# Performance work log

Hardware: AMD Instinct MI355X
Metric: run time of the kernel (lower is better)

Reference implementation:

```python
import jax, jax.numpy as jnp
import numpy as np

NUM_USER = 20000
NUM_ITEM = 40000
N_NODES = NUM_USER + NUM_ITEM
DIM = 64
V_DIM = 2048
T_DIM = 768
N_EDGES = 1_000_000
K_USER = 40
K_ITEM = 10
N_LAYERS = 2


def setup_inputs() -> dict:
    key = jax.random.key(0)
    ks = iter(jax.random.split(key, 32))

    def xavier(shape):
        s = (2.0 / (shape[0] + shape[-1])) ** 0.5
        return jax.random.normal(next(ks), shape, jnp.float32) * s

    # bipartite user-item interactions, doubled (undirected), as in DRAGON.__init__
    u = jax.random.randint(next(ks), (N_EDGES,), 0, NUM_USER)
    it = jax.random.randint(next(ks), (N_EDGES,), NUM_USER, N_NODES)
    edge_index = jnp.stack([jnp.concatenate([u, it]), jnp.concatenate([it, u])])

    v_feat = jax.random.normal(next(ks), (NUM_ITEM, V_DIM), jnp.float32)
    t_feat = jax.random.normal(next(ks), (NUM_ITEM, T_DIM), jnp.float32)

    # KNN item-item adjacency (top-10 per row) with symmetric-normalized values,
    # mirroring get_knn_adj_mat/compute_normalized_laplacian
    rows = jnp.repeat(jnp.arange(NUM_ITEM), K_ITEM)
    cols = jax.random.randint(next(ks), (NUM_ITEM * K_ITEM,), 0, NUM_ITEM)
    mm_indices = jnp.stack([rows, cols])
    row_sum = jax.ops.segment_sum(jnp.ones(NUM_ITEM * K_ITEM, jnp.float32), rows,
                                  num_segments=NUM_ITEM) + 1e-7
    rinv = row_sum ** -0.5
    mm_values = rinv[rows] * rinv[cols]

    user_graph = jax.random.randint(next(ks), (NUM_USER, K_USER), 0, NUM_USER)
    user_weight_matrix = jax.nn.softmax(
        jax.random.normal(next(ks), (NUM_USER, K_USER), jnp.float32), axis=1)
    weight_u = jax.nn.softmax(
        jax.random.normal(next(ks), (NUM_USER, 2, 1), jnp.float32), axis=1)

    return {
        'edge_index': edge_index,
        'v_feat': v_feat, 't_feat': t_feat,
        'v_pref': xavier((NUM_USER, DIM)), 't_pref': xavier((NUM_USER, DIM)),
        'v_mlp1_w': xavier((V_DIM, 4 * DIM)), 'v_mlp1_b': jnp.zeros(4 * DIM, jnp.float32),
        'v_mlp2_w': xavier((4 * DIM, DIM)), 'v_mlp2_b': jnp.zeros(DIM, jnp.float32),
        't_mlp1_w': xavier((T_DIM, 4 * DIM)), 't_mlp1_b': jnp.zeros(4 * DIM, jnp.float32),
        't_mlp2_w': xavier((4 * DIM, DIM)), 't_mlp2_b': jnp.zeros(DIM, jnp.float32),
        'v_conv_w': xavier((DIM, DIM)), 'v_conv_b': jnp.zeros(DIM, jnp.float32),
        't_conv_w': xavier((DIM, DIM)), 't_conv_b': jnp.zeros(DIM, jnp.float32),
        'weight_u': weight_u,
        'user_graph': user_graph,
        'user_weight_matrix': user_weight_matrix,
        'mm_indices': mm_indices,
        'mm_values': mm_values,
    }


def _l2n(x):
    n = jnp.linalg.norm(x, axis=-1, keepdims=True)
    return x / jnp.maximum(n, 1e-12)


def reference(edge_index, v_feat, t_feat, v_pref, t_pref,
              v_mlp1_w, v_mlp1_b, v_mlp2_w, v_mlp2_b,
              t_mlp1_w, t_mlp1_b, t_mlp2_w, t_mlp2_b,
              v_conv_w, v_conv_b, t_conv_w, t_conv_b,
              weight_u, user_graph, user_weight_matrix,
              mm_indices, mm_values):
    seg = jax.ops.segment_sum
    # GCNConv normalization with self-loops (shared by both branches)
    sl = jnp.arange(N_NODES)
    src = jnp.concatenate([edge_index[0], sl])
    dst = jnp.concatenate([edge_index[1], sl])
    deg = seg(jnp.ones_like(dst, dtype=jnp.float32), dst, num_segments=N_NODES)
    dinv = deg ** -0.5
    norm = (dinv[src] * dinv[dst])[:, None]

    def conv(x, w, b):  # out[dst] += norm * (x @ w)[src], then bias
        return seg(norm * (x @ w)[src], dst, num_segments=N_NODES) + b

    def branch(feat, pref, w1, b1, w2, b2, cw, cb):
        temp = jax.nn.leaky_relu(feat @ w1 + b1) @ w2 + b2  # [I, D]
        x = _l2n(jnp.concatenate([pref, temp], axis=0))      # [N, D]
        h = conv(x, cw, cb)
        h1 = conv(h, cw, cb)
        return x + h + h1

    v_rep = branch(v_feat, v_pref, v_mlp1_w, v_mlp1_b, v_mlp2_w, v_mlp2_b, v_conv_w, v_conv_b)
    t_rep = branch(t_feat, t_pref, t_mlp1_w, t_mlp1_b, t_mlp2_w, t_mlp2_b, t_conv_w, t_conv_b)

    representation = jnp.concatenate([v_rep, t_rep], axis=1)  # [N, 2D]
    wu = weight_u[:, :, 0]  # [U, 2]
    user_rep = jnp.concatenate([wu[:, 0:1] * v_rep[:NUM_USER],
                                wu[:, 1:2] * t_rep[:NUM_USER]], axis=1)  # [U, 2D]
    item_rep = representation[NUM_USER:]  # [I, 2D]

    # User_Graph_sample: weighted sum over sampled user neighborhoods
    h_u = jnp.einsum('uk,ukd->ud', user_weight_matrix, user_rep[user_graph])
    user_rep = user_rep + h_u

    # n_layers of sparse Laplacian propagation over KNN item-item graph
    row, col = mm_indices[0], mm_indices[1]
    h_i = item_rep
    for _ in range(N_LAYERS):
        h_i = seg(mm_values[:, None] * h_i[col], row, num_segments=NUM_ITEM)
    item_rep = item_rep + h_i

    return jnp.concatenate([user_rep, item_rep], axis=0)  # [N, 2D]
```

## Files before the change

### kernel.cpp

```cpp
#include <hip/hip_runtime.h>

#define NUSER 20000
#define NITEM 40000
#define NNODE 60000
#define DIM   64
#define NE    1000000
#define KUSER 40
#define KITEM 10

typedef __attribute__((ext_vector_type(8))) short short8v;
typedef __attribute__((ext_vector_type(4))) float floatx4;

__device__ inline short bf16rne(float f) {
    unsigned u = __builtin_bit_cast(unsigned, f);
    unsigned r = (u + 0x7fffu + ((u >> 16) & 1u)) >> 16;
    return (short)r;
}
__device__ inline unsigned cvt_pk_bf16(float lo, float hi) {
    unsigned r;
    asm("v_cvt_pk_bf16_f32 %0, %1, %2" : "=v"(r) : "v"(lo), "v"(hi));
    return r;
}
__device__ inline float bflo(unsigned v) { return __builtin_bit_cast(float, v << 16); }
__device__ inline float bfhi(unsigned v) { return __builtin_bit_cast(float, v & 0xffff0000u); }

#define CNTB ((NE + 255) / 256)
#define TRB  2944
__global__ __launch_bounds__(256) void k_count_transpose(const int* __restrict__ uu, const int* __restrict__ it,
                                                         int* __restrict__ cnt,
                                                         const float* __restrict__ W1v, const float* __restrict__ W1t,
                                                         const float* __restrict__ W2v, const float* __restrict__ W2t,
                                                         short* __restrict__ Bv, short* __restrict__ Bt,
                                                         short* __restrict__ B2v, short* __restrict__ B2t) {
    __shared__ float s[16][17];
    int bid = blockIdx.x;
    if (bid < CNTB) {
        int i = bid * 256 + threadIdx.x;
        if (i >= NE) return;
        atomicAdd(&cnt[uu[i]], 1);
        atomicAdd(&cnt[it[i]], 1);
        return;
    }
    bid -= CNTB;
    const float* B; short* D; int K, N, local;
    if (bid < 2048)      { B = W1v; D = Bv;  K = 2048; N = 256; local = bid; }
    else if (bid < 2816) { B = W1t; D = Bt;  K = 768;  N = 256; local = bid - 2048; }
    else if (bid < 2880) { B = W2v; D = B2v; K = 256;  N = 64;  local = bid - 2816; }
    else                 { B = W2t; D = B2t; K = 256;  N = 64;  local = bid - 2880; }
    int ktiles = K >> 4;
    int k0 = (local % ktiles) * 16, n0 = (local / ktiles) * 16;
    int t = threadIdx.x, tx = t & 15, ty = t >> 4;
    s[ty][tx] = B[(size_t)(k0 + ty) * N + n0 + tx];
    __syncthreads();
    int k = k0 + tx, n = n0 + ty;
    D[(size_t)(k >> 5) * (N * 32) + n * 32 + (k & 31)] = bf16rne(s[tx][ty]);
}

__global__ __launch_bounds__(256) void k_scanA(const int* __restrict__ v, int* __restrict__ excl,
                                               int* __restrict__ bsum, float* __restrict__ dinv, int n) {
    __shared__ int s[256];
    int t = threadIdx.x, i = blockIdx.x * 256 + t;
    int orig = (i < n) ? v[i] : 0;
    if (i < n) dinv[i] = 1.0f / sqrtf((float)(orig + 1));
    s[t] = orig; __syncthreads();
    #pragma unroll
    for (int off = 1; off < 256; off <<= 1) {
        int u = (t >= off) ? s[t - off] : 0;
        __syncthreads();
        s[t] += u;
        __syncthreads();
    }
    if (i < n) excl[i] = s[t] - orig;
    if (t == 255) bsum[blockIdx.x] = s[255];
}

__global__ __launch_bounds__(256) void k_scanB_prep(int* __restrict__ bsum, int nb,
                                                    const float* __restrict__ Wv, const float* __restrict__ Wt,
                                                    const float* __restrict__ bv, const float* __restrict__ bt,
                                                    short* __restrict__ Bcat, float* __restrict__ bw,
                                                    float* __restrict__ bb) {
    __shared__ float Wld[2][64][65];
    __shared__ float W2ld[2][64][65];
    int t = threadIdx.x;
    if (blockIdx.x == 0) {
        int* s = (int*)&Wld[0][0][0];
        int orig = (t < nb) ? bsum[t] : 0;
        s[t] = orig; __syncthreads();
        #pragma unroll
        for (int off = 1; off < 256; off <<= 1) {
            int u = (t >= off) ? s[t - off] : 0;
            __syncthreads();
            s[t] += u;
            __syncthreads();
        }
        if (t < nb) bsum[t] = s[t] - orig;
        return;
    }
    for (int id = t; id < 8192; id += 256) {
        int z = id >> 12, k = (id >> 6) & 63, n = id & 63;
        Wld[z][k][n] = (z ? Wt : Wv)[k * 64 + n];
    }
    __syncthreads();
    for (int id = t; id < 8192; id += 256) {
        int z = id >> 12, k = (id >> 6) & 63, n = id & 63;
        float a = 0.f;
        #pragma unroll 8
        for (int m = 0; m < 64; m++) a += Wld[z][k][m] * Wld[z][m][n];
        W2ld[z][k][n] = a;
    }
    __syncthreads();
    for (int id = t; id < 32768; id += 256) {
        int k = id >> 7, n = id & 127;
        int kb = k >> 6, kk = k & 63;
        float v = 0.f;
        if (kb == 0)      { if (n < 64)  v = Wld[0][kk][n]; }
        else if (kb == 1) { if (n >= 64) v = Wld[1][kk][n - 64]; }
        else if (kb == 2) { if (n < 64)  v = W2ld[0][kk][n]; }
        else              { if (n >= 64) v = W2ld[1][kk][n - 64]; }
        Bcat[(k >> 5) * 4096 + n * 32 + (k & 31)] = bf16rne(v);
    }
    if (t < 128) {
        int z = t >> 6, n = t & 63;
        const float* b = z ? bt : bv;
        float a = 0.f;
        #pragma unroll 8
        for (int k = 0; k < 64; k++) a += b[k] * Wld[z][k][n];
        bw[t] = a;
        bb[t] = 2.f * b[n];
    }
}

__global__ __launch_bounds__(256) void k_scanC(int* __restrict__ excl, const int* __restrict__ bsum,
                                               int* __restrict__ cursor, int n) {
    int i = blockIdx.x * 256 + threadIdx.x;
    if (i < n) {
        int v = excl[i] + bsum[blockIdx.x];
        excl[i] = v;
        cursor[i] = v;
    }
    if (i == 0) excl[n] = 2 * NE;
}

#define AP   40
#define MIDP 264
#define MBLK 128
#define VBLKS ((NITEM + MBLK - 1) / MBLK)
#define FILLB ((NE + 511) / 512)
#define MLPB  (2 * VBLKS)
#define L2NB  (NUSER * 2 / 8)
__global__ __launch_bounds__(512, 4) void k_fill_mlp_l2n(
        const int* __restrict__ uu, const int* __restrict__ it, const float* __restrict__ dinv,
        int* __restrict__ cursor, unsigned* __restrict__ csr_pkd,
        const float* __restrict__ Av, const float* __restrict__ At,
        const short* __restrict__ B1v, const short* __restrict__ B1t,
        const float* __restrict__ b1v, const float* __restrict__ b1t,
        const short* __restrict__ B2v, const short* __restrict__ B2t,
        const float* __restrict__ b2v, const float* __restrict__ b2t,
        const float* __restrict__ prefv, const float* __restrict__ preft,
        unsigned* __restrict__ xbf) {
    __shared__ short smem[MBLK * MIDP];
    const int tid = threadIdx.x;
    int bid = blockIdx.x;

    if (bid < FILLB) {
        int i = bid * 512 + tid;
        if (i >= NE) return;
        int u = uu[i], t = it[i];
        unsigned pku = ((unsigned)(unsigned short)bf16rne(dinv[u]) << 16) | (unsigned)u;
        unsigned pkt = ((unsigned)(unsigned short)bf16rne(dinv[t]) << 16) | (unsigned)t;
        int pos1 = atomicAdd(&cursor[t], 1);
        csr_pkd[pos1] = pku;
        int pos2 = atomicAdd(&cursor[u], 1);
        csr_pkd[pos2] = pkt;
        return;
    }
    bid -= FILLB;

    if (bid >= MLPB) {
        int lb = bid - MLPB;
        int lane = tid & 63;
        int wg = lb * 8 + (tid >> 6);
        int row = wg >> 1, br = wg & 1;
        if (row >= NUSER) return;
        const float* p = br ? preft : prefv;
        float v = p[(size_t)row * 64 + lane];
        float ss = v * v;
        #pragma unroll
        for (int off = 32; off >= 1; off >>= 1) ss += __shfl_xor(ss, off, 64);
        float xn = v / fmaxf(sqrtf(ss), 1e-12f);
        float pn = __shfl_xor(xn, 1, 64);
        if (!(lane & 1))
            xbf[(size_t)row * 64 + (br ? 32 : 0) + (lane >> 1)] = cvt_pk_bf16(xn, pn);
        return;
    }

    short* As = smem;
    short* Bs = smem + 2 * MBLK * AP;
    const bool isV = bid < VBLKS;
    const float* A    = isV ? Av : At;
    const short* B1t_ = isV ? B1v : B1t;
    const float* b1   = isV ? b1v : b1t;
    const short* B2t_ = isV ? B2v : B2t;
    const float* b2   = isV ? b2v : b2t;
    const int K = isV ? 2048 : 768;
    const int boff = isV ? 0 : 32;
    const int rowBase = (isV ? bid : bid - VBLKS) * MBLK;

    const int lane = tid & 63, wid = tid >> 6;
    const int wr = wid >> 2, wc = wid & 3;

    const int sar = tid >> 2, sac = (tid & 3) * 8;
    int aclamp = rowBase + sar; if (aclamp > NITEM - 1) aclamp = NITEM - 1;
    const float* aptr = A + (size_t)aclamp * K + sac;

    const int fk = (lane >> 4) * 8;
    const int faoff = (wr * 64 + (lane & 15)) * AP + fk;
    const int fboff = (wc * 64 + (lane & 15)) * AP + fk;

    floatx4 acc[4][4];
    #pragma unroll
    for (int m = 0; m < 4; m++)
        #pragma unroll
        for (int n = 0; n < 4; n++) acc[m][n] = (floatx4)0.f;

    float4 ra0, ra1;
    short8v rb0, rb1;
    const int nk = K >> 5;

    auto ldg = [&](int ks) {
        const float* ap = aptr + ks * 32;
        ra0 = *(const float4*)(ap);
        ra1 = *(const float4*)(ap + 4);
        const short* bsrc = B1t_ + (size_t)ks * 8192 + tid * 16;
        rb0 = *(const short8v*)(bsrc);
        rb1 = *(const short8v*)(bsrc + 8);
    };
    auto stv = [&](int buf) {
        uint4 av;
        av.x = cvt_pk_bf16(ra0.x, ra0.y); av.y = cvt_pk_bf16(ra0.z, ra0.w);
        av.z = cvt_pk_bf16(ra1.x, ra1.y); av.w = cvt_pk_bf16(ra1.z, ra1.w);
        *(uint4*)&As[buf * (MBLK * AP) + sar * AP + sac] = av;
        short* bd = &Bs[buf * (256 * AP) + (tid >> 1) * AP + (tid & 1) * 16];
        *(short8v*)(bd) = rb0;
        *(short8v*)(bd + 8) = rb1;
    };

    ldg(0); stv(0);
    __syncthreads();
    int cur = 0;
    for (int ks = 0; ks < nk; ++ks) {
        if (ks + 1 < nk) ldg(ks + 1);
        short8v a[4], b[4];
        #pragma unroll
        for (int m = 0; m < 4; m++) a[m] = *(const short8v*)&As[cur * (MBLK * AP) + faoff + m * 16 * AP];
        #pragma unroll
        for (int n = 0; n < 4; n++) b[n] = *(const short8v*)&Bs[cur * (256 * AP) + fboff + n * 16 * AP];
        #pragma unroll
        for (int m = 0; m < 4; m++)
            #pragma unroll
            for (int n = 0; n < 4; n++)
                acc[m][n] = __builtin_amdgcn_mfma_f32_16x16x32_bf16(a[m], b[n], acc[m][n], 0, 0, 0);
        if (ks + 1 < nk) stv(cur ^ 1);
        __syncthreads();
        cur ^= 1;
    }

    unsigned* mid32 = (unsigned*)smem;
    float bcol[4];
    #pragma unroll
    for (int n = 0; n < 4; n++) bcol[n] = b1[wc * 64 + n * 16 + (lane & 15)];
    #pragma unroll
    for (int m = 0; m < 4; m++)
        #pragma unroll
        for (int n = 0; n < 4; n++) {
            int col = wc * 64 + n * 16 + (lane & 15);
            #pragma unroll
            for (int q = 0; q < 4; q++) {
                int row = wr * 64 + m * 16 + (lane >> 4) * 4 + q;
                float v = acc[m][n][q] + bcol[n];
                v = v > 0.f ? v : 0.01f * v;
                float pn = __shfl_xor(v, 1, 64);
                if (!(lane & 1)) mid32[row * 132 + (col >> 1)] = cvt_pk_bf16(v, pn);
            }
        }
    __syncthreads();

    const short* mid = smem;
    floatx4 acc2[4];
    #pragma unroll
    for (int n2 = 0; n2 < 4; n2++) acc2[n2] = (floatx4)0.f;
    const int arow = wid * 16 + (lane & 15);
    #pragma unroll
    for (int ks2 = 0; ks2 < 8; ++ks2) {
        short8v af = *(const short8v*)&mid[arow * MIDP + ks2 * 32 + fk];
        const short* bp = B2t_ + ks2 * 2048 + fk;
        short8v bf4[4];
        #pragma unroll
        for (int n2 = 0; n2 < 4; n2++) bf4[n2] = *(const short8v*)(bp + (n2 * 16 + (lane & 15)) * 32);
        #pragma unroll
        for (int n2 = 0; n2 < 4; n2++)
            acc2[n2] = __builtin_amdgcn_mfma_f32_16x16x32_bf16(af, bf4[n2], acc2[n2], 0, 0, 0);
    }

    float b2c[4];
    #pragma unroll
    for (int n2 = 0; n2 < 4; n2++) b2c[n2] = b2[n2 * 16 + (lane & 15)];
    #pragma unroll
    for (int q = 0; q < 4; ++q) {
        float v[4]; float ss = 0.f;
        #pragma unroll
        for (int n2 = 0; n2 < 4; n2++) { v[n2] = acc2[n2][q] + b2c[n2]; ss += v[n2] * v[n2]; }
        ss += __shfl_xor(ss, 1, 64);
        ss += __shfl_xor(ss, 2, 64);
        ss += __shfl_xor(ss, 4, 64);
        ss += __shfl_xor(ss, 8, 64);
        float sc = 1.f / fmaxf(sqrtf(ss), 1e-12f);
        int lr = wid * 16 + (lane >> 4) * 4 + q;
        int grow = NUSER + rowBase + lr;
        bool ok = (rowBase + lr) < NITEM;
        #pragma unroll
        for (int n2 = 0; n2 < 4; n2++) {
            float xn = v[n2] * sc;
            float pn = __shfl_xor(xn, 1, 64);
            if (ok && !(lane & 1))
                xbf[(size_t)grow * 64 + boff + n2 * 8 + ((lane & 15) >> 1)] = cvt_pk_bf16(xn, pn);
        }
    }
}

__global__ __launch_bounds__(256) void k_gather_p(const int* __restrict__ rowptr, const unsigned* __restrict__ csr_pkd,
                                                  const float* __restrict__ dinv, const unsigned* __restrict__ in_bf,
                                                  unsigned* __restrict__ out_bf, float* __restrict__ s_out) {
    int row = blockIdx.x * 4 + (threadIdx.x >> 6);
    int lane = threadIdx.x & 63;
    if (row >= NNODE) return;
    int p0 = rowptr[row], p1 = rowptr[row + 1];
    float dr = dinv[row];
    unsigned sv = in_bf[(size_t)row * 64 + lane];
    float ax0 = dr * bflo(sv), ay0 = dr * bfhi(sv);
    float ax1 = 0.f, ay1 = 0.f;
    float wsum = 0.f;
    for (int p = p0; p < p1; p += 64) {
        int c = p1 - p; if (c > 64) c = 64;
        unsigned pk = (lane < c) ? csr_pkd[p + lane] : 0u;
        wsum += bfhi(pk);
        int j = 0;
        for (; j + 4 <= c; j += 4) {
            unsigned e0 = __shfl(pk, j, 64),     e1 = __shfl(pk, j + 1, 64);
            unsigned e2 = __shfl(pk, j + 2, 64), e3 = __shfl(pk, j + 3, 64);
            unsigned v0 = in_bf[(size_t)(e0 & 0xffffu) * 64 + lane];
            unsigned v1 = in_bf[(size_t)(e1 & 0xffffu) * 64 + lane];
            unsigned v2 = in_bf[(size_t)(e2 & 0xffffu) * 64 + lane];
            unsigned v3 = in_bf[(size_t)(e3 & 0xffffu) * 64 + lane];
            float w0 = bfhi(e0), w1 = bfhi(e1), w2 = bfhi(e2), w3 = bfhi(e3);
            ax0 += w0 * bflo(v0); ay0 += w0 * bfhi(v0);
            ax1 += w1 * bflo(v1); ay1 += w1 * bfhi(v1);
            ax0 += w2 * bflo(v2); ay0 += w2 * bfhi(v2);
            ax1 += w3 * bflo(v3); ay1 += w3 * bfhi(v3);
        }
        for (; j < c; ++j) {
            unsigned e = __shfl(pk, j, 64);
            unsigned v = in_bf[(size_t)(e & 0xffffu) * 64 + lane];
            float w = bfhi(e);
            ax0 += w * bflo(v); ay0 += w * bfhi(v);
        }
    }
    out_bf[(size_t)row * 64 + lane] = cvt_pk_bf16(dr * (ax0 + ax1), dr * (ay0 + ay1));
    #pragma unroll
    for (int o = 32; o >= 1; o >>= 1) wsum += __shfl_xor(wsum, o, 64);
    if (lane == 0) s_out[row] = dr * (dr + wsum);
}

__global__ __launch_bounds__(512) void k_gather2_rep(const int* __restrict__ rowptr, const unsigned* __restrict__ csr_pkd,
                                                     const float* __restrict__ dinv, const unsigned* __restrict__ g1,
                                                     const short* __restrict__ Bcat, const unsigned* __restrict__ x_bf,
                                                     const float* __restrict__ s, const float* __restrict__ bw,
                                                     const float* __restrict__ bb, const float* __restrict__ weight_u,
                                                     float* __restrict__ rep0, unsigned* __restrict__ rep_bf) {
    __shared__ short As[16 * 264];
    const int tid = threadIdx.x, lane = tid & 63, w = tid >> 6;
    const int rowBase = blockIdx.x * 16;

    for (int rr = 0; rr < 2; ++rr) {
        int lrow = w * 2 + rr;
        int row = rowBase + lrow;
        int p0 = rowptr[row], p1 = rowptr[row + 1];
        float dr = dinv[row];
        unsigned sv = g1[(size_t)row * 64 + lane];
        float ax0 = dr * bflo(sv), ay0 = dr * bfhi(sv);
        float ax1 = 0.f, ay1 = 0.f;
        for (int p = p0; p < p1; p += 64) {
            int c = p1 - p; if (c > 64) c = 64;
            unsigned pk = (lane < c) ? csr_pkd[p + lane] : 0u;
            int j = 0;
            for (; j + 4 <= c; j += 4) {
                unsigned e0 = __shfl(pk, j, 64),     e1 = __shfl(pk, j + 1, 64);
                unsigned e2 = __shfl(pk, j + 2, 64), e3 = __shfl(pk, j + 3, 64);
                unsigned v0 = g1[(size_t)(e0 & 0xffffu) * 64 + lane];
                unsigned v1 = g1[(size_t)(e1 & 0xffffu) * 64 + lane];
                unsigned v2 = g1[(size_t)(e2 & 0xffffu) * 64 + lane];
                unsigned v3 = g1[(size_t)(e3 & 0xffffu) * 64 + lane];
                float w0 = bfhi(e0), w1 = bfhi(e1), w2 = bfhi(e2), w3 = bfhi(e3);
                ax0 += w0 * bflo(v0); ay0 += w0 * bfhi(v0);
                ax1 += w1 * bflo(v1); ay1 += w1 * bfhi(v1);
                ax0 += w2 * bflo(v2); ay0 += w2 * bfhi(v2);
                ax1 += w3 * bflo(v3); ay1 += w3 * bfhi(v3);
            }
            for (; j < c; ++j) {
                unsigned e = __shfl(pk, j, 64);
                unsigned v = g1[(size_t)(e & 0xffffu) * 64 + lane];
                float wj = bfhi(e);
                ax0 += wj * bflo(v); ay0 += wj * bfhi(v);
            }
        }
        *(unsigned*)&As[lrow * 264 + 2 * lane] = sv;
        *(unsigned*)&As[lrow * 264 + 128 + 2 * lane] = cvt_pk_bf16(dr * (ax0 + ax1), dr * (ay0 + ay1));
    }
    __syncthreads();

    const int fk = (lane >> 4) * 8;
    floatx4 acc = (floatx4)0.f;
    #pragma unroll
    for (int ks = 0; ks < 8; ++ks) {
        short8v af = *(const short8v*)&As[(lane & 15) * 264 + ks * 32 + fk];
        short8v bf = *(const short8v*)(Bcat + ks * 4096 + (w * 16 + (lane & 15)) * 32 + fk);
        acc = __builtin_amdgcn_mfma_f32_16x16x32_bf16(af, bf, acc, 0, 0, 0);
    }
    const int col = w * 16 + (lane & 15);
    const float bwc = bw[col], bbc = bb[col];
    #pragma unroll
    for (int q = 0; q < 4; ++q) {
        int lrow = (lane >> 4) * 4 + q;
        int row = rowBase + lrow;
        unsigned xw = x_bf[(size_t)row * 64 + (col >> 1)];
        float xval = (col & 1) ? bfhi(xw) : bflo(xw);
        float v = acc[q] + xval + s[row] * bwc + bbc;
        float wu = (row < NUSER) ? weight_u[row * 2 + (col >> 6)] : 1.0f;
        v *= wu;
        rep0[(size_t)row * 128 + col] = v;
        float pn = __shfl_xor(v, 1, 64);
        if (!(lane & 1))
            rep_bf[(size_t)row * 64 + (col >> 1)] = cvt_pk_bf16(v, pn);
    }
}

#define UBLK (NUSER * 64 / 256)
__global__ __launch_bounds__(256) void k_user_item1(const float* __restrict__ rep0, const unsigned* __restrict__ rep_bf,
                                                    const int* __restrict__ ug, const float* __restrict__ uwm,
                                                    const int* __restrict__ mm_col, const float* __restrict__ mm_values,
                                                    float* __restrict__ out, unsigned* __restrict__ tmp_bf) {
    int bid = blockIdx.x;
    if (bid < UBLK) {
        int id = bid * 256 + threadIdx.x;
        int u = id >> 6, lane = id & 63;
        float2 acc = *(const float2*)(rep0 + (size_t)u * 128 + 2 * lane);
        #pragma unroll 4
        for (int k = 0; k < KUSER; k++) {
            int nb = ug[u * KUSER + k];
            float w = uwm[u * KUSER + k];
            unsigned v = rep_bf[(size_t)nb * 64 + lane];
            acc.x += w * bflo(v);
            acc.y += w * bfhi(v);
        }
        *(float2*)(out + (size_t)u * 128 + 2 * lane) = acc;
    } else {
        int id = (bid - UBLK) * 256 + threadIdx.x;
        int r = id >> 6, lane = id & 63;
        float ax = 0.f, ay = 0.f;
        #pragma unroll
        for (int j = 0; j < KITEM; j++) {
            int c = mm_col[r * KITEM + j];
            float w = mm_values[r * KITEM + j];
            unsigned v = rep_bf[(size_t)(NUSER + c) * 64 + lane];
            ax += w * bflo(v);
            ay += w * bfhi(v);
        }
        tmp_bf[(size_t)r * 64 + lane] = cvt_pk_bf16(ax, ay);
    }
}

__global__ __launch_bounds__(256) void k_item2(const float* __restrict__ rep0, const unsigned* __restrict__ tmp_bf,
                                               const int* __restrict__ mm_col, const float* __restrict__ mm_values,
                                               float* __restrict__ out) {
    int id = blockIdx.x * 256 + threadIdx.x;
    int r = id >> 6, lane = id & 63;
    if (r >= NITEM) return;
    float ax = 0.f, ay = 0.f;
    #pragma unroll
    for (int j = 0; j < KITEM; j++) {
        int c = mm_col[r * KITEM + j];
        float w = mm_values[r * KITEM + j];
        unsigned v = tmp_bf[(size_t)c * 64 + lane];
        ax += w * bflo(v);
        ay += w * bfhi(v);
    }
    float2 base = *(const float2*)(rep0 + (size_t)(NUSER + r) * 128 + 2 * lane);
    float2 o;
    o.x = base.x + ax;
    o.y = base.y + ay;
    *(float2*)(out + (size_t)(NUSER + r) * 128 + 2 * lane) = o;
}

extern "C" void kernel_launch(void* const* d_in, const int* in_sizes, int n_in,
                              void* d_out, int out_size, void* d_ws, size_t ws_size,
                              hipStream_t stream) {
    const int*   edge_index = (const int*)d_in[0];
    const float* v_feat   = (const float*)d_in[1];
    const float* t_feat   = (const float*)d_in[2];
    const float* v_pref   = (const float*)d_in[3];
    const float* t_pref   = (const float*)d_in[4];
    const float* v_mlp1_w = (const float*)d_in[5];
    const float* v_mlp1_b = (const float*)d_in[6];
    const float* v_mlp2_w = (const float*)d_in[7];
    const float* v_mlp2_b = (const float*)d_in[8];
    const float* t_mlp1_w = (const float*)d_in[9];
    const float* t_mlp1_b = (const float*)d_in[10];
    const float* t_mlp2_w = (const float*)d_in[11];
    const float* t_mlp2_b = (const float*)d_in[12];
    const float* v_conv_w = (const float*)d_in[13];
    const float* v_conv_b = (const float*)d_in[14];
    const float* t_conv_w = (const float*)d_in[15];
    const float* t_conv_b = (const float*)d_in[16];
    const float* weight_u = (const float*)d_in[17];
    const int*   user_graph = (const int*)d_in[18];
    const float* uwm      = (const float*)d_in[19];
    const int*   mm_indices = (const int*)d_in[20];
    const float* mm_values  = (const float*)d_in[21];
    float* out = (float*)d_out;

    char* wsb = (char*)d_ws;
    size_t off = 0;
    auto alloc = [&](size_t bytes) -> void* {
        void* p = wsb + off;
        off = (off + bytes + 255) & ~(size_t)255;
        return p;
    };
    int*      cnt     = (int*)     alloc(NNODE * 4);
    float*    dinv    = (float*)   alloc(NNODE * 4);
    int*      rowptr  = (int*)     alloc((NNODE + 1) * 4);
    int*      bsum    = (int*)     alloc(256 * 4);
    int*      cursor  = (int*)     alloc(NNODE * 4);
    unsigned* csr_pkd = (unsigned*)alloc((size_t)2 * NE * 4);
    short*    Btw_v   = (short*)   alloc((size_t)2048 * 256 * 2);
    short*    Btw_t   = (short*)   alloc((size_t)768 * 256 * 2);
    short*    W2b_v   = (short*)   alloc((size_t)256 * 64 * 2);
    short*    W2b_t   = (short*)   alloc((size_t)256 * 64 * 2);
    short*    Bcat    = (short*)   alloc((size_t)256 * 128 * 2);
    float*    bw      = (float*)   alloc(128 * 4);
    float*    bb      = (float*)   alloc(128 * 4);
    float*    svec    = (float*)   alloc(NNODE * 4);
    unsigned* x_bf    = (unsigned*)alloc((size_t)NNODE * 64 * 4);
    unsigned* g1      = (unsigned*)alloc((size_t)NNODE * 64 * 4);
    float*    rep0    = (float*)   alloc((size_t)NNODE * 128 * 4);
    unsigned* rep_bf  = (unsigned*)alloc((size_t)NNODE * 64 * 4);
    unsigned* tmp_bf  = (unsigned*)alloc((size_t)NITEM * 64 * 4);
    (void)ws_size; (void)n_in; (void)in_sizes; (void)out_size;

    const int* pairs_u  = edge_index;
    const int* pairs_it = edge_index + NE;
    const int* mm_col = mm_indices + NITEM * KITEM;

    const int NB = (NNODE + 255) / 256;

    hipMemsetAsync(cnt, 0, NNODE * 4, stream);
    k_count_transpose<<<CNTB + TRB, 256, 0, stream>>>(pairs_u, pairs_it, cnt,
                                                      v_mlp1_w, t_mlp1_w, v_mlp2_w, t_mlp2_w,
                                                      Btw_v, Btw_t, W2b_v, W2b_t);
    k_scanA<<<NB, 256, 0, stream>>>(cnt, rowptr, bsum, dinv, NNODE);
    k_scanB_prep<<<2, 256, 0, stream>>>(bsum, NB, v_conv_w, t_conv_w, v_conv_b, t_conv_b, Bcat, bw, bb);
    k_scanC<<<NB, 256, 0, stream>>>(rowptr, bsum, cursor, NNODE);

    k_fill_mlp_l2n<<<FILLB + MLPB + L2NB, 512, 0, stream>>>(
        pairs_u, pairs_it, dinv, cursor, csr_pkd,
        v_feat, t_feat, Btw_v, Btw_t, v_mlp1_b, t_mlp1_b,
        W2b_v, W2b_t, v_mlp2_b, t_mlp2_b, v_pref, t_pref, x_bf);

    k_gather_p<<<(NNODE + 3) / 4, 256, 0, stream>>>(rowptr, csr_pkd, dinv, x_bf, g1, svec);
    k_gather2_rep<<<NNODE / 16, 512, 0, stream>>>(rowptr, csr_pkd, dinv, g1, Bcat, x_bf,
                                                  svec, bw, bb, weight_u, rep0, rep_bf);

    k_user_item1<<<UBLK + NITEM * 64 / 256, 256, 0, stream>>>(rep0, rep_bf, user_graph, uwm,
                                                              mm_col, mm_values, out, tmp_bf);
    k_item2<<<NITEM * 64 / 256, 256, 0, stream>>>(rep0, tmp_bf, mm_col, mm_values, out);
}
```

Measured before the change: 559.1 us.

## Split fill from MLP kernel, move l2n into count kernel, deepen prefetch

Moves the user-preference L2-normalisation blocks into the earlier count/transpose kernel and splits the CSR fill out of the fused MLP kernel into its own launch. The MLP GEMM main loop now prefetches global loads two k-steps ahead instead of one, holding an extra set of staging registers. The intent is to hide more global-load latency in the MLP and stop the atomic-heavy fill blocks from sharing a launch with the GEMM blocks. In exchange it adds a kernel launch, serialises fill before the MLP, and raises register pressure in the GEMM.

```diff
diff --git a/kernel.cpp b/kernel.cpp
--- a/kernel.cpp
+++ b/kernel.cpp
@@ -26,12 +26,15 @@
 
 #define CNTB ((NE + 255) / 256)
 #define TRB  2944
-__global__ __launch_bounds__(256) void k_count_transpose(const int* __restrict__ uu, const int* __restrict__ it,
-                                                         int* __restrict__ cnt,
-                                                         const float* __restrict__ W1v, const float* __restrict__ W1t,
-                                                         const float* __restrict__ W2v, const float* __restrict__ W2t,
-                                                         short* __restrict__ Bv, short* __restrict__ Bt,
-                                                         short* __restrict__ B2v, short* __restrict__ B2t) {
+#define L2NB (NUSER * 2 / 4)
+__global__ __launch_bounds__(256) void k_count_transpose_l2n(
+        const int* __restrict__ uu, const int* __restrict__ it, int* __restrict__ cnt,
+        const float* __restrict__ W1v, const float* __restrict__ W1t,
+        const float* __restrict__ W2v, const float* __restrict__ W2t,
+        short* __restrict__ Bv, short* __restrict__ Bt,
+        short* __restrict__ B2v, short* __restrict__ B2t,
+        const float* __restrict__ prefv, const float* __restrict__ preft,
+        unsigned* __restrict__ xbf) {
     __shared__ float s[16][17];
     int bid = blockIdx.x;
     if (bid < CNTB) {
@@ -42,6 +45,23 @@
         return;
     }
     bid -= CNTB;
+    if (bid >= TRB) {
+        int lb = bid - TRB;
+        int lane = threadIdx.x & 63;
+        int wg = lb * 4 + (threadIdx.x >> 6);
+        int row = wg >> 1, br = wg & 1;
+        if (row >= NUSER) return;
+        const float* p = br ? preft : prefv;
+        float v = p[(size_t)row * 64 + lane];
+        float ss = v * v;
+        #pragma unroll
+        for (int off = 32; off >= 1; off >>= 1) ss += __shfl_xor(ss, off, 64);
+        float xn = v / fmaxf(sqrtf(ss), 1e-12f);
+        float pn = __shfl_xor(xn, 1, 64);
+        if (!(lane & 1))
+            xbf[(size_t)row * 64 + (br ? 32 : 0) + (lane >> 1)] = cvt_pk_bf16(xn, pn);
+        return;
+    }
     const float* B; short* D; int K, N, local;
     if (bid < 2048)      { B = W1v; D = Bv;  K = 2048; N = 256; local = bid; }
     else if (bid < 2816) { B = W1t; D = Bt;  K = 768;  N = 256; local = bid - 2048; }
@@ -141,62 +161,34 @@
     if (i == 0) excl[n] = 2 * NE;
 }
 
+__global__ __launch_bounds__(256) void k_fill_pair(const int* __restrict__ uu, const int* __restrict__ it,
+                                                   const float* __restrict__ dinv, int* __restrict__ cursor,
+                                                   unsigned* __restrict__ csr_pkd) {
+    int i = blockIdx.x * 256 + threadIdx.x;
+    if (i >= NE) return;
+    int u = uu[i], t = it[i];
+    unsigned pku = ((unsigned)(unsigned short)bf16rne(dinv[u]) << 16) | (unsigned)u;
+    unsigned pkt = ((unsigned)(unsigned short)bf16rne(dinv[t]) << 16) | (unsigned)t;
+    int pos1 = atomicAdd(&cursor[t], 1);
+    csr_pkd[pos1] = pku;
+    int pos2 = atomicAdd(&cursor[u], 1);
+    csr_pkd[pos2] = pkt;
+}
+
 #define AP   40
 #define MIDP 264
 #define MBLK 128
 #define VBLKS ((NITEM + MBLK - 1) / MBLK)
-#define FILLB ((NE + 511) / 512)
-#define MLPB  (2 * VBLKS)
-#define L2NB  (NUSER * 2 / 8)
-__global__ __launch_bounds__(512, 4) void k_fill_mlp_l2n(
-        const int* __restrict__ uu, const int* __restrict__ it, const float* __restrict__ dinv,
-        int* __restrict__ cursor, unsigned* __restrict__ csr_pkd,
-        const float* __restrict__ Av, const float* __restrict__ At,
-        const short* __restrict__ B1v, const short* __restrict__ B1t,
-        const float* __restrict__ b1v, const float* __restrict__ b1t,
-        const short* __restrict__ B2v, const short* __restrict__ B2t,
-        const float* __restrict__ b2v, const float* __restrict__ b2t,
-        const float* __restrict__ prefv, const float* __restrict__ preft,
-        unsigned* __restrict__ xbf) {
+__global__ __launch_bounds__(512, 4) void mlp_merged(const float* __restrict__ Av, const float* __restrict__ At,
+                                                  const short* __restrict__ B1v, const short* __restrict__ B1t,
+                                                  const float* __restrict__ b1v, const float* __restrict__ b1t,
+                                                  const short* __restrict__ B2v, const short* __restrict__ B2t,
+                                                  const float* __restrict__ b2v, const float* __restrict__ b2t,
+                                                  unsigned* __restrict__ xbf) {
     __shared__ short smem[MBLK * MIDP];
-    const int tid = threadIdx.x;
-    int bid = blockIdx.x;
-
-    if (bid < FILLB) {
-        int i = bid * 512 + tid;
-        if (i >= NE) return;
-        int u = uu[i], t = it[i];
-        unsigned pku = ((unsigned)(unsigned short)bf16rne(dinv[u]) << 16) | (unsigned)u;
-        unsigned pkt = ((unsigned)(unsigned short)bf16rne(dinv[t]) << 16) | (unsigned)t;
-        int pos1 = atomicAdd(&cursor[t], 1);
-        csr_pkd[pos1] = pku;
-        int pos2 = atomicAdd(&cursor[u], 1);
-        csr_pkd[pos2] = pkt;
-        return;
-    }
-    bid -= FILLB;
-
-    if (bid >= MLPB) {
-        int lb = bid - MLPB;
-        int lane = tid & 63;
-        int wg = lb * 8 + (tid >> 6);
-        int row = wg >> 1, br = wg & 1;
-        if (row >= NUSER) return;
-        const float* p = br ? preft : prefv;
-        float v = p[(size_t)row * 64 + lane];
-        float ss = v * v;
-        #pragma unroll
-        for (int off = 32; off >= 1; off >>= 1) ss += __shfl_xor(ss, off, 64);
-        float xn = v / fmaxf(sqrtf(ss), 1e-12f);
-        float pn = __shfl_xor(xn, 1, 64);
-        if (!(lane & 1))
-            xbf[(size_t)row * 64 + (br ? 32 : 0) + (lane >> 1)] = cvt_pk_bf16(xn, pn);
-        return;
-    }
-
     short* As = smem;
     short* Bs = smem + 2 * MBLK * AP;
-    const bool isV = bid < VBLKS;
+    const bool isV = blockIdx.x < VBLKS;
     const float* A    = isV ? Av : At;
     const short* B1t_ = isV ? B1v : B1t;
     const float* b1   = isV ? b1v : b1t;
@@ -204,8 +196,9 @@
     const float* b2   = isV ? b2v : b2t;
     const int K = isV ? 2048 : 768;
     const int boff = isV ? 0 : 32;
-    const int rowBase = (isV ? bid : bid - VBLKS) * MBLK;
-
+    const int rowBase = (isV ? blockIdx.x : blockIdx.x - VBLKS) * MBLK;
+
+    const int tid = threadIdx.x;
     const int lane = tid & 63, wid = tid >> 6;
     const int wr = wid >> 2, wc = wid & 3;
 
@@ -223,33 +216,35 @@
         #pragma unroll
         for (int n = 0; n < 4; n++) acc[m][n] = (floatx4)0.f;
 
-    float4 ra0, ra1;
-    short8v rb0, rb1;
+    float4 ra0, ra1; short8v rb0, rb1;
+    float4 na0, na1; short8v nb0, nb1;
     const int nk = K >> 5;
 
-    auto ldg = [&](int ks) {
+    auto ldgT = [&](int ks, float4& a0, float4& a1, short8v& b0, short8v& b1) {
         const float* ap = aptr + ks * 32;
-        ra0 = *(const float4*)(ap);
-        ra1 = *(const float4*)(ap + 4);
+        a0 = *(const float4*)(ap);
+        a1 = *(const float4*)(ap + 4);
         const short* bsrc = B1t_ + (size_t)ks * 8192 + tid * 16;
-        rb0 = *(const short8v*)(bsrc);
-        rb1 = *(const short8v*)(bsrc + 8);
+        b0 = *(const short8v*)(bsrc);
+        b1 = *(const short8v*)(bsrc + 8);
     };
-    auto stv = [&](int buf) {
+    auto stvT = [&](int buf, const float4& a0, const float4& a1, const short8v& b0, const short8v& b1) {
         uint4 av;
-        av.x = cvt_pk_bf16(ra0.x, ra0.y); av.y = cvt_pk_bf16(ra0.z, ra0.w);
-        av.z = cvt_pk_bf16(ra1.x, ra1.y); av.w = cvt_pk_bf16(ra1.z, ra1.w);
+        av.x = cvt_pk_bf16(a0.x, a0.y); av.y = cvt_pk_bf16(a0.z, a0.w);
+        av.z = cvt_pk_bf16(a1.x, a1.y); av.w = cvt_pk_bf16(a1.z, a1.w);
         *(uint4*)&As[buf * (MBLK * AP) + sar * AP + sac] = av;
         short* bd = &Bs[buf * (256 * AP) + (tid >> 1) * AP + (tid & 1) * 16];
-        *(short8v*)(bd) = rb0;
-        *(short8v*)(bd + 8) = rb1;
+        *(short8v*)(bd) = b0;
+        *(short8v*)(bd + 8) = b1;
     };
 
-    ldg(0); stv(0);
+    ldgT(0, ra0, ra1, rb0, rb1);
+    stvT(0, ra0, ra1, rb0, rb1);
     __syncthreads();
+    ldgT(1, ra0, ra1, rb0, rb1);
     int cur = 0;
     for (int ks = 0; ks < nk; ++ks) {
-        if (ks + 1 < nk) ldg(ks + 1);
+        if (ks + 2 < nk) ldgT(ks + 2, na0, na1, nb0, nb1);
         short8v a[4], b[4];
         #pragma unroll
         for (int m = 0; m < 4; m++) a[m] = *(const short8v*)&As[cur * (MBLK * AP) + faoff + m * 16 * AP];
@@ -260,8 +255,9 @@
             #pragma unroll
             for (int n = 0; n < 4; n++)
                 acc[m][n] = __builtin_amdgcn_mfma_f32_16x16x32_bf16(a[m], b[n], acc[m][n], 0, 0, 0);
-        if (ks + 1 < nk) stv(cur ^ 1);
+        if (ks + 1 < nk) stvT(cur ^ 1, ra0, ra1, rb0, rb1);
         __syncthreads();
+        ra0 = na0; ra1 = na1; rb0 = nb0; rb1 = nb1;
         cur ^= 1;
     }
 
@@ -563,17 +559,16 @@
     const int NB = (NNODE + 255) / 256;
 
     hipMemsetAsync(cnt, 0, NNODE * 4, stream);
-    k_count_transpose<<<CNTB + TRB, 256, 0, stream>>>(pairs_u, pairs_it, cnt,
-                                                      v_mlp1_w, t_mlp1_w, v_mlp2_w, t_mlp2_w,
-                                                      Btw_v, Btw_t, W2b_v, W2b_t);
+    k_count_transpose_l2n<<<CNTB + TRB + L2NB, 256, 0, stream>>>(
+        pairs_u, pairs_it, cnt, v_mlp1_w, t_mlp1_w, v_mlp2_w, t_mlp2_w,
+        Btw_v, Btw_t, W2b_v, W2b_t, v_pref, t_pref, x_bf);
     k_scanA<<<NB, 256, 0, stream>>>(cnt, rowptr, bsum, dinv, NNODE);
     k_scanB_prep<<<2, 256, 0, stream>>>(bsum, NB, v_conv_w, t_conv_w, v_conv_b, t_conv_b, Bcat, bw, bb);
     k_scanC<<<NB, 256, 0, stream>>>(rowptr, bsum, cursor, NNODE);
 
-    k_fill_mlp_l2n<<<FILLB + MLPB + L2NB, 512, 0, stream>>>(
-        pairs_u, pairs_it, dinv, cursor, csr_pkd,
-        v_feat, t_feat, Btw_v, Btw_t, v_mlp1_b, t_mlp1_b,
-        W2b_v, W2b_t, v_mlp2_b, t_mlp2_b, v_pref, t_pref, x_bf);
+    k_fill_pair<<<(NE + 255) / 256, 256, 0, stream>>>(pairs_u, pairs_it, dinv, cursor, csr_pkd);
+    mlp_merged<<<2 * VBLKS, 512, 0, stream>>>(v_feat, t_feat, Btw_v, Btw_t, v_mlp1_b, t_mlp1_b,
+                                              W2b_v, W2b_t, v_mlp2_b, t_mlp2_b, x_bf);
 
     k_gather_p<<<(NNODE + 3) / 4, 256, 0, stream>>>(rowptr, csr_pkd, dinv, x_bf, g1, svec);
     k_gather2_rep<<<NNODE / 16, 512, 0, stream>>>(rowptr, csr_pkd, dinv, g1, Bcat, x_bf,
```

New measurement: 564.2 us (median of 2 runs). Within noise of the previous version (+0.9%).
